# Kernel optimization log

Measured on AMD Instinct MI355X. Metric: run time of the kernel, lower is better.

The kernel has to match this reference:

```python
import jax, jax.numpy as jnp
import numpy as np

N_WINDOW = 128  # |i-j| < N_WINDOW kept
D_K = 64

def setup_inputs() -> dict:
    key = jax.random.key(0)
    kq, kk, kv = jax.random.split(key, 3)
    B, H, S, D = 2, 8, 2048, D_K
    Q = jax.random.normal(kq, (B, H, S, D), dtype=jnp.float32)
    K = jax.random.normal(kk, (B, H, S, D), dtype=jnp.float32)
    V = jax.random.normal(kv, (B, H, S, D), dtype=jnp.float32)
    return {"Q": Q, "K": K, "V": V}

def reference(Q, K, V):
    S = Q.shape[-2]
    # scores: [B, H, S, S]
    scores = jnp.einsum('bhqd,bhkd->bhqk', Q, K) / jnp.sqrt(jnp.float32(D_K))
    idx = jnp.arange(S)
    band = jnp.abs(idx[:, None] - idx[None, :]) < N_WINDOW  # [S, S] band mask
    scores = jnp.where(band[None, None, :, :], scores, -jnp.inf)
    attn = jax.nn.softmax(scores, axis=-1)
    context = jnp.einsum('bhqk,bhkd->bhqd', attn, V)
    return (context, attn)
```

## Files before the change

### kernel.cpp

```cpp
#include <hip/hip_runtime.h>
#include <hip/hip_bf16.h>
#include <math.h>

#define S_LEN 2048
#define DK 64
#define TQ 32
#define KLW 320
#define NCH 5
#define PSTR 324
#define PSTR4 81

typedef __attribute__((ext_vector_type(8))) short bf16x8;
typedef __attribute__((ext_vector_type(4))) float f32x4;

__device__ __forceinline__ bf16x8 pack8(f32x4 a, f32x4 b) {
    union { __hip_bfloat162 h[4]; bf16x8 v; } u;
    u.h[0] = __float22bfloat162_rn(make_float2(a[0], a[1]));
    u.h[1] = __float22bfloat162_rn(make_float2(a[2], a[3]));
    u.h[2] = __float22bfloat162_rn(make_float2(b[0], b[1]));
    u.h[3] = __float22bfloat162_rn(make_float2(b[2], b[3]));
    return u.v;
}

__global__ __launch_bounds__(256, 3) void band_attn_v7(
    const float* __restrict__ Q,
    const float* __restrict__ K,
    const float* __restrict__ V,
    float* __restrict__ ctx_out,
    float* __restrict__ attn_out)
{
    __shared__ __align__(16) float Ps[TQ * PSTR];

    const int tid  = threadIdx.x;
    const int bh   = blockIdx.x >> 6;
    const int q0   = (blockIdx.x & 63) * TQ;
    const int base = q0 - 128;
    const int cls  = blockIdx.x & 1;

    const int lane = tid & 63;
    const int wv   = tid >> 6;
    const int col  = lane & 15;
    const int quad = lane >> 4;

    const float* Qh = Q + ((size_t)bh * S_LEN + q0) * DK;
    const float* Kh = K + (size_t)bh * S_LEN * DK;
    const float* Vh = V + (size_t)bh * S_LEN * DK;

    const int kloff4 = (q0 >> 2) - 32;
    const int L = max(0, kloff4);
    const int R = min(512, kloff4 + (KLW >> 2));
    f32x4* A4w = (f32x4*)(attn_out + ((size_t)bh * S_LEN + q0 + 8 * wv) * S_LEN);

    auto store_zeros = [&]() {
        const f32x4 z = {0.f, 0.f, 0.f, 0.f};
        #pragma unroll
        for (int rr = 0; rr < 8; ++rr) {
            f32x4* row4 = A4w + (size_t)rr * 512;
            for (int s = lane; s < L; s += 64)
                __builtin_nontemporal_store(z, row4 + s);
            for (int s = R + lane; s < 512; s += 64)
                __builtin_nontemporal_store(z, row4 + s);
        }
    };

    bf16x8 qf[2][2];
    #pragma unroll
    for (int qt = 0; qt < 2; ++qt)
        #pragma unroll
        for (int h = 0; h < 2; ++h) {
            const float* qp = Qh + (size_t)(16 * qt + col) * DK + 32 * h + 8 * quad;
            f32x4 a = *(const f32x4*)qp;
            f32x4 b = *(const f32x4*)(qp + 4);
            a *= 0.125f; b *= 0.125f;
            qf[qt][h] = pack8(a, b);
        }

    #pragma unroll
    for (int c = 0; c < NCH; ++c) {
        const int kl  = c * 64 + 16 * wv + col;
        const int kg  = base + kl;
        const int kgc = min(max(kg, 0), S_LEN - 1);
        bf16x8 kf[2];
        #pragma unroll
        for (int h = 0; h < 2; ++h) {
            const float* kp = Kh + (size_t)kgc * DK + 32 * h + 8 * quad;
            kf[h] = pack8(*(const f32x4*)kp, *(const f32x4*)(kp + 4));
        }
        #pragma unroll
        for (int qt = 0; qt < 2; ++qt) {
            f32x4 acc = {0.f, 0.f, 0.f, 0.f};
            acc = __builtin_amdgcn_mfma_f32_16x16x32_bf16(qf[qt][0], kf[0], acc, 0, 0, 0);
            acc = __builtin_amdgcn_mfma_f32_16x16x32_bf16(qf[qt][1], kf[1], acc, 0, 0, 0);
            #pragma unroll
            for (int r = 0; r < 4; ++r) {
                const int qloc = 16 * qt + quad * 4 + r;
                const bool ok = ((unsigned)kg < S_LEN) && (kl > qloc) && (kl <= qloc + 255);
                Ps[qloc * PSTR + kl] = ok ? acc[r] : -INFINITY;
            }
        }
    }

    if (cls) store_zeros();
    __syncthreads();

    #pragma unroll
    for (int rr = 0; rr < 8; ++rr) {
        float* row = Ps + (wv * 8 + rr) * PSTR;
        float v[5];
        #pragma unroll
        for (int j = 0; j < 5; ++j) v[j] = row[lane + 64 * j];
        float m = fmaxf(fmaxf(fmaxf(v[0], v[1]), fmaxf(v[2], v[3])), v[4]);
        #pragma unroll
        for (int off = 32; off > 0; off >>= 1) m = fmaxf(m, __shfl_xor(m, off, 64));
        float e[5], sum = 0.f;
        #pragma unroll
        for (int j = 0; j < 5; ++j) { e[j] = __expf(v[j] - m); sum += e[j]; }
        #pragma unroll
        for (int off = 32; off > 0; off >>= 1) sum += __shfl_xor(sum, off, 64);
        const float inv = 1.0f / sum;
        float* arow = attn_out + ((size_t)bh * S_LEN + q0 + 8 * wv + rr) * S_LEN;
        #pragma unroll
        for (int j = 0; j < 5; ++j) {
            const float p = e[j] * inv;
            row[lane + 64 * j] = p;
            const int kg = base + lane + 64 * j;
            if ((unsigned)kg < S_LEN)
                __builtin_nontemporal_store(p, arow + kg);
        }
    }
    __syncthreads();

    f32x4 o0 = {0.f, 0.f, 0.f, 0.f}, o1 = {0.f, 0.f, 0.f, 0.f};
    const float* vcol = Vh + 16 * wv + col;
    #pragma unroll
    for (int c = 0; c < NCH; ++c) {
        #pragma unroll
        for (int h = 0; h < 2; ++h) {
            const int k0 = base + c * 64 + 32 * h + 8 * quad;
            f32x4 va, vb;
            #pragma unroll
            for (int j = 0; j < 4; ++j) {
                int kgc = min(max(k0 + j, 0), S_LEN - 1);
                va[j] = vcol[(size_t)kgc * DK];
            }
            #pragma unroll
            for (int j = 0; j < 4; ++j) {
                int kgc = min(max(k0 + 4 + j, 0), S_LEN - 1);
                vb[j] = vcol[(size_t)kgc * DK];
            }
            bf16x8 vf = pack8(va, vb);
            #pragma unroll
            for (int qt = 0; qt < 2; ++qt) {
                const float* pp = Ps + (size_t)(16 * qt + col) * PSTR + c * 64 + 32 * h + 8 * quad;
                bf16x8 pf = pack8(*(const f32x4*)pp, *(const f32x4*)(pp + 4));
                if (qt == 0) o0 = __builtin_amdgcn_mfma_f32_16x16x32_bf16(pf, vf, o0, 0, 0, 0);
                else         o1 = __builtin_amdgcn_mfma_f32_16x16x32_bf16(pf, vf, o1, 0, 0, 0);
            }
        }
    }

    {
        float* Cg = ctx_out + ((size_t)bh * S_LEN + q0) * DK;
        #pragma unroll
        for (int r = 0; r < 4; ++r) {
            Cg[(size_t)(quad * 4 + r) * DK + 16 * wv + col]      = o0[r];
            Cg[(size_t)(16 + quad * 4 + r) * DK + 16 * wv + col] = o1[r];
        }
    }

    if (!cls) store_zeros();
}

extern "C" void kernel_launch(void* const* d_in, const int* in_sizes, int n_in,
                              void* d_out, int out_size, void* d_ws, size_t ws_size,
                              hipStream_t stream) {
    const float* Q = (const float*)d_in[0];
    const float* K = (const float*)d_in[1];
    const float* V = (const float*)d_in[2];
    float* out = (float*)d_out;

    const int BH = in_sizes[0] / (S_LEN * DK);
    const size_t ctx_elems = (size_t)BH * S_LEN * DK;
    float* ctx  = out;
    float* attn = out + ctx_elems;

    dim3 grid(BH * (S_LEN / TQ));
    band_attn_v7<<<grid, 256, 0, stream>>>(Q, K, V, ctx, attn);
}
```

Baseline: 297.7 us.

## Swizzle score tile in LDS and write full attention rows as aligned float4 stores

The padded shared-memory row stride is replaced by an XOR swizzle on columns, so the tile is smaller and bank conflicts are still avoided. This allows raising launch bounds to four blocks per CU. The separate zero-fill pass and the scalar probability stores are merged into one loop per row that writes all 512 float4 chunks with nontemporal stores, taking band values from LDS and zeros elsewhere. The aim is full-width vectorized writes of the large attention output, at the cost of more index arithmetic, and it depends on the band window being aligned to float4 boundaries.

```diff
diff --git a/kernel.cpp b/kernel.cpp
--- a/kernel.cpp
+++ b/kernel.cpp
@@ -7,8 +7,7 @@
 #define TQ 32
 #define KLW 320
 #define NCH 5
-#define PSTR 324
-#define PSTR4 81
+#define PSTR 320
 
 typedef __attribute__((ext_vector_type(8))) short bf16x8;
 typedef __attribute__((ext_vector_type(4))) float f32x4;
@@ -22,7 +21,8 @@
     return u.v;
 }
 
-__global__ __launch_bounds__(256, 3) void band_attn_v7(
+
+__global__ __launch_bounds__(256, 4) void band_attn_v8(
     const float* __restrict__ Q,
     const float* __restrict__ K,
     const float* __restrict__ V,
@@ -35,7 +35,6 @@
     const int bh   = blockIdx.x >> 6;
     const int q0   = (blockIdx.x & 63) * TQ;
     const int base = q0 - 128;
-    const int cls  = blockIdx.x & 1;
 
     const int lane = tid & 63;
     const int wv   = tid >> 6;
@@ -45,23 +44,6 @@
     const float* Qh = Q + ((size_t)bh * S_LEN + q0) * DK;
     const float* Kh = K + (size_t)bh * S_LEN * DK;
     const float* Vh = V + (size_t)bh * S_LEN * DK;
-
-    const int kloff4 = (q0 >> 2) - 32;
-    const int L = max(0, kloff4);
-    const int R = min(512, kloff4 + (KLW >> 2));
-    f32x4* A4w = (f32x4*)(attn_out + ((size_t)bh * S_LEN + q0 + 8 * wv) * S_LEN);
-
-    auto store_zeros = [&]() {
-        const f32x4 z = {0.f, 0.f, 0.f, 0.f};
-        #pragma unroll
-        for (int rr = 0; rr < 8; ++rr) {
-            f32x4* row4 = A4w + (size_t)rr * 512;
-            for (int s = lane; s < L; s += 64)
-                __builtin_nontemporal_store(z, row4 + s);
-            for (int s = R + lane; s < 512; s += 64)
-                __builtin_nontemporal_store(z, row4 + s);
-        }
-    };
 
     bf16x8 qf[2][2];
     #pragma unroll
@@ -95,20 +77,22 @@
             for (int r = 0; r < 4; ++r) {
                 const int qloc = 16 * qt + quad * 4 + r;
                 const bool ok = ((unsigned)kg < S_LEN) && (kl > qloc) && (kl <= qloc + 255);
-                Ps[qloc * PSTR + kl] = ok ? acc[r] : -INFINITY;
+                Ps[qloc * PSTR + (kl ^ ((qloc & 7) << 2))] = ok ? acc[r] : -INFINITY;
             }
         }
     }
 
-    if (cls) store_zeros();
     __syncthreads();
 
+    const int W0 = (q0 >> 2) - 32;
     #pragma unroll
     for (int rr = 0; rr < 8; ++rr) {
-        float* row = Ps + (wv * 8 + rr) * PSTR;
+        const int qrow = 8 * wv + rr;
+        float* row = Ps + qrow * PSTR;
+        const int Cq = (qrow & 7) << 2;
         float v[5];
         #pragma unroll
-        for (int j = 0; j < 5; ++j) v[j] = row[lane + 64 * j];
+        for (int j = 0; j < 5; ++j) v[j] = row[(lane + 64 * j) ^ Cq];
         float m = fmaxf(fmaxf(fmaxf(v[0], v[1]), fmaxf(v[2], v[3])), v[4]);
         #pragma unroll
         for (int off = 32; off > 0; off >>= 1) m = fmaxf(m, __shfl_xor(m, off, 64));
@@ -118,41 +102,50 @@
         #pragma unroll
         for (int off = 32; off > 0; off >>= 1) sum += __shfl_xor(sum, off, 64);
         const float inv = 1.0f / sum;
-        float* arow = attn_out + ((size_t)bh * S_LEN + q0 + 8 * wv + rr) * S_LEN;
         #pragma unroll
-        for (int j = 0; j < 5; ++j) {
-            const float p = e[j] * inv;
-            row[lane + 64 * j] = p;
-            const int kg = base + lane + 64 * j;
-            if ((unsigned)kg < S_LEN)
-                __builtin_nontemporal_store(p, arow + kg);
+        for (int j = 0; j < 5; ++j)
+            row[(lane + 64 * j) ^ Cq] = e[j] * inv;
+
+        f32x4* arow4 = (f32x4*)(attn_out + ((size_t)bh * S_LEN + q0 + qrow) * S_LEN);
+        #pragma unroll
+        for (int it = 0; it < 8; ++it) {
+            const int s = lane + 64 * it;
+            const int d = s - W0;
+            f32x4 p4 = {0.f, 0.f, 0.f, 0.f};
+            if ((unsigned)d < 80u)
+                p4 = *(const f32x4*)(row + ((4 * d) ^ Cq));
+            __builtin_nontemporal_store(p4, arow4 + s);
         }
     }
     __syncthreads();
 
     f32x4 o0 = {0.f, 0.f, 0.f, 0.f}, o1 = {0.f, 0.f, 0.f, 0.f};
     const float* vcol = Vh + 16 * wv + col;
+    const int Cr = (col & 7) << 2;
     #pragma unroll
     for (int c = 0; c < NCH; ++c) {
         #pragma unroll
         for (int h = 0; h < 2; ++h) {
-            const int k0 = base + c * 64 + 32 * h + 8 * quad;
+            const int k0l = c * 64 + 32 * h + 8 * quad;
+            const int k0g = base + k0l;
             f32x4 va, vb;
             #pragma unroll
             for (int j = 0; j < 4; ++j) {
-                int kgc = min(max(k0 + j, 0), S_LEN - 1);
+                int kgc = min(max(k0g + j, 0), S_LEN - 1);
                 va[j] = vcol[(size_t)kgc * DK];
             }
             #pragma unroll
             for (int j = 0; j < 4; ++j) {
-                int kgc = min(max(k0 + 4 + j, 0), S_LEN - 1);
+                int kgc = min(max(k0g + 4 + j, 0), S_LEN - 1);
                 vb[j] = vcol[(size_t)kgc * DK];
             }
             bf16x8 vf = pack8(va, vb);
             #pragma unroll
             for (int qt = 0; qt < 2; ++qt) {
-                const float* pp = Ps + (size_t)(16 * qt + col) * PSTR + c * 64 + 32 * h + 8 * quad;
-                bf16x8 pf = pack8(*(const f32x4*)pp, *(const f32x4*)(pp + 4));
+                const float* prow = Ps + (size_t)(16 * qt + col) * PSTR;
+                f32x4 a = *(const f32x4*)(prow + (k0l ^ Cr));
+                f32x4 b = *(const f32x4*)(prow + ((k0l + 4) ^ Cr));
+                bf16x8 pf = pack8(a, b);
                 if (qt == 0) o0 = __builtin_amdgcn_mfma_f32_16x16x32_bf16(pf, vf, o0, 0, 0, 0);
                 else         o1 = __builtin_amdgcn_mfma_f32_16x16x32_bf16(pf, vf, o1, 0, 0, 0);
             }
@@ -167,8 +160,6 @@
             Cg[(size_t)(16 + quad * 4 + r) * DK + 16 * wv + col] = o1[r];
         }
     }
-
-    if (!cls) store_zeros();
 }
 
 extern "C" void kernel_launch(void* const* d_in, const int* in_sizes, int n_in,
@@ -185,5 +176,5 @@
     float* attn = out + ctx_elems;
 
     dim3 grid(BH * (S_LEN / TQ));
-    band_attn_v7<<<grid, 256, 0, stream>>>(Q, K, V, ctx, attn);
+    band_attn_v8<<<grid, 256, 0, stream>>>(Q, K, V, ctx, attn);
 }
```

Measured after the change: 298.1 us. No clear change (+0.2%).
